# Kernel optimization log

Measured on AMD Instinct MI355X. Metric: run time of the kernel, lower is better.

The kernel has to match this reference:

```python
import jax, jax.numpy as jnp
import numpy as np

NORM_S = 3.0  # normalize_scale, learn_scale=False
NUM_CLASSES = 32


def setup_inputs() -> dict:
    key = jax.random.key(0)
    k1, k2 = jax.random.split(key)
    x = jax.random.normal(k1, (512, 128), dtype=jnp.float32)
    labels = jax.random.randint(k2, (512,), 0, NUM_CLASSES, dtype=jnp.int64)
    return {"x": x, "labels": labels}


def reference(x, labels):
    # L2-normalize rows and scale (MyTripletLoss.forward)
    f = NORM_S * x / jnp.linalg.norm(x, axis=1, keepdims=True)
    # pairwise squared distances, clamped at 0 (pairwise_distances)
    sq = jnp.sum(f * f, axis=1)
    D = jnp.clip(sq[:, None] + sq[None, :] - 2.0 * (f @ f.T), 0.0, None)  # [N,N]
    N = x.shape[0]
    # triplet_type == 0: valid triplet (i,j,k) iff i!=j, l_i==l_j, l_i!=l_k
    same = (labels[:, None] == labels[None, :]) & (~jnp.eye(N, dtype=bool))  # [i,j]
    diff = labels[:, None] != labels[None, :]                                # [i,k]
    mask = same[:, :, None] & diff[:, None, :]                               # [i,j,k]
    # DBL loss: log(1 + exp(D_ij - D_ik)) = softplus
    lt = jax.nn.softplus(D[:, :, None] - D[:, None, :])                      # [i,j,k]
    triplet_count = jnp.sum(mask).astype(lt.dtype)
    loss = jnp.sum(jnp.where(mask, lt, 0.0)) / triplet_count
    return loss.reshape(1)
```

## Files before the change

kernel.cpp:

```cpp
#include <hip/hip_runtime.h>
#include <math.h>

#define N 512
#define DIM 128
#define TT 32
#define PADS 132
#define NTRI (16 * 17 / 2)


__global__ void __launch_bounds__(256) gram_kernel(const float* __restrict__ x,
                                                   float* __restrict__ D) {
    __shared__ float xi[TT * PADS];
    __shared__ float xj[TT * PADS];
    __shared__ float rnA[TT];
    __shared__ float rnB[TT];

    int t = threadIdx.x;

    int b = blockIdx.x;
    int bi = (int)((sqrtf(8.0f * (float)b + 1.0f) - 1.0f) * 0.5f);
    while ((bi + 1) * (bi + 2) / 2 <= b) ++bi;
    while (bi * (bi + 1) / 2 > b) --bi;
    int bj = b - bi * (bi + 1) / 2;

    const float4* srcA = (const float4*)(x + bi * TT * DIM);
    const float4* srcB = (const float4*)(x + bj * TT * DIM);
    #pragma unroll
    for (int k = 0; k < (TT * DIM / 4) / 256; ++k) {
        int e = t + k * 256;
        int r = e >> 5, c4 = e & 31;
        *((float4*)(xi + r * PADS + 4 * c4)) = srcA[e];
        *((float4*)(xj + r * PADS + 4 * c4)) = srcB[e];
    }
    __syncthreads();

    {
        int quart = t & 3, r = t >> 2;
        const float* base = (r < TT) ? (xi + r * PADS) : (xj + (r - TT) * PADS);
        const float4* a = (const float4*)(base + quart * 32);
        float s0 = 0.0f, s1 = 0.0f;
        #pragma unroll
        for (int q = 0; q < 8; q += 2) {
            float4 a0 = a[q], a1 = a[q + 1];
            s0 += a0.x * a0.x + a0.y * a0.y + a0.z * a0.z + a0.w * a0.w;
            s1 += a1.x * a1.x + a1.y * a1.y + a1.z * a1.z + a1.w * a1.w;
        }
        float ss = s0 + s1;
        ss += __shfl_xor(ss, 1, 64);
        ss += __shfl_xor(ss, 2, 64);
        if (quart == 0) {
            if (r < TT) rnA[r] = rsqrtf(ss);
            else        rnB[r - TT] = rsqrtf(ss);
        }
    }
    __syncthreads();

    int tx = t & 15, ty = t >> 4;
    int i0 = 2 * ty, i1 = i0 + 1, j0 = 2 * tx, j1 = j0 + 1;
    float acc00 = 0.0f, acc01 = 0.0f, acc10 = 0.0f, acc11 = 0.0f;
    const float4* A0 = (const float4*)(xi + i0 * PADS);
    const float4* A1 = (const float4*)(xi + i1 * PADS);
    const float4* B0 = (const float4*)(xj + j0 * PADS);
    const float4* B1 = (const float4*)(xj + j1 * PADS);
    #pragma unroll 8
    for (int k4 = 0; k4 < DIM / 4; ++k4) {
        float4 a0 = A0[k4], a1 = A1[k4], b0 = B0[k4], b1 = B1[k4];
        acc00 += a0.x * b0.x + a0.y * b0.y + a0.z * b0.z + a0.w * b0.w;
        acc01 += a0.x * b1.x + a0.y * b1.y + a0.z * b1.z + a0.w * b1.w;
        acc10 += a1.x * b0.x + a1.y * b0.y + a1.z * b0.z + a1.w * b0.w;
        acc11 += a1.x * b1.x + a1.y * b1.y + a1.z * b1.z + a1.w * b1.w;
    }
    float ri0 = rnA[i0], ri1 = rnA[i1], rj0 = rnB[j0], rj1 = rnB[j1];
    float t00 = 18.0f * fmaxf(0.0f, 1.0f - acc00 * ri0 * rj0);
    float t01 = 18.0f * fmaxf(0.0f, 1.0f - acc01 * ri0 * rj1);
    float t10 = 18.0f * fmaxf(0.0f, 1.0f - acc10 * ri1 * rj0);
    float t11 = 18.0f * fmaxf(0.0f, 1.0f - acc11 * ri1 * rj1);

    {
        int gi0 = bi * TT + i0, gi1 = bi * TT + i1, gj = bj * TT + j0;
        float2 r0 = {t00, t01}, r1 = {t10, t11};
        *((float2*)(D + gi0 * N + gj)) = r0;
        *((float2*)(D + gi1 * N + gj)) = r1;
    }

    if (bi != bj) {
        __syncthreads();
        float* Tt = xi;
        Tt[j0 * 33 + i0] = t00;
        Tt[j1 * 33 + i0] = t01;
        Tt[j0 * 33 + i1] = t10;
        Tt[j1 * 33 + i1] = t11;
        __syncthreads();
        int ga0 = bj * TT + i0, ga1 = bj * TT + i1, gb = bi * TT + j0;
        float2 m0 = {Tt[i0 * 33 + j0], Tt[i0 * 33 + j1]};
        float2 m1 = {Tt[i1 * 33 + j0], Tt[i1 * 33 + j1]};
        *((float2*)(D + ga0 * N + gb)) = m0;
        *((float2*)(D + ga1 * N + gb)) = m1;
    }
}

__global__ void __launch_bounds__(256) loss_kernel(const float* __restrict__ Dm,
                                                   const int* __restrict__ labels,
                                                   float* __restrict__ sums,
                                                   float* __restrict__ cnts) {
    __shared__ int   lab[N];
    __shared__ float sameD[N];
    __shared__ float diffD[N];
    __shared__ float red[4];
    __shared__ int   nsame, ndiff;

    int i = blockIdx.x, t = threadIdx.x;
    lab[t]       = labels[t];
    lab[t + 256] = labels[t + 256];
    if (t == 0) { nsame = 0; ndiff = 0; }
    float d0 = Dm[i * N + t];
    float d1 = Dm[i * N + t + 256];
    __syncthreads();

    int li = lab[i];
    {
        int j = t;
        if (lab[j] == li) {
            if (j != i) { int p = atomicAdd(&nsame, 1); sameD[p] = d0; }
        } else { int p = atomicAdd(&ndiff, 1); diffD[p] = d0; }
        j = t + 256;
        if (lab[j] == li) {
            if (j != i) { int p = atomicAdd(&nsame, 1); sameD[p] = d1; }
        } else { int p = atomicAdd(&ndiff, 1); diffD[p] = d1; }
    }
    __syncthreads();

    int ns = nsame, nd = ndiff;
    float ek0 = (t < nd)       ? __expf(-diffD[t])       : 0.0f;
    float ek1 = (t + 256 < nd) ? __expf(-diffD[t + 256]) : 0.0f;
    float lsum = 0.0f;
    for (int js = 0; js < ns; ++js) {
        float es = __expf(sameD[js]);
        lsum += __logf(1.0f + es * ek0) + __logf(1.0f + es * ek1);
    }

    #pragma unroll
    for (int off = 32; off > 0; off >>= 1) lsum += __shfl_xor(lsum, off, 64);
    if ((t & 63) == 0) red[t >> 6] = lsum;
    __syncthreads();
    if (t == 0) {
        sums[i] = red[0] + red[1] + red[2] + red[3];
        cnts[i] = (float)(ns * nd);
    }
}

__global__ void __launch_bounds__(256) finalize_kernel(const float* __restrict__ sums,
                                                       const float* __restrict__ cnts,
                                                       float* __restrict__ out) {
    __shared__ float2 red[256];
    int t = threadIdx.x;
    float2 v;
    v.x = sums[t] + sums[t + 256];
    v.y = cnts[t] + cnts[t + 256];
    red[t] = v;
    __syncthreads();
    #pragma unroll
    for (int s = 128; s > 0; s >>= 1) {
        if (t < s) {
            red[t].x += red[t + s].x;
            red[t].y += red[t + s].y;
        }
        __syncthreads();
    }
    if (t == 0) out[0] = red[0].x / red[0].y;
}

extern "C" void kernel_launch(void* const* d_in, const int* in_sizes, int n_in,
                              void* d_out, int out_size, void* d_ws, size_t ws_size,
                              hipStream_t stream) {
    const float* x      = (const float*)d_in[0];
    const int*   labels = (const int*)d_in[1];
    float*       out    = (float*)d_out;

    float* Dm   = (float*)d_ws;
    float* sums = Dm + N * N;
    float* cnts = sums + N;

    gram_kernel<<<NTRI, 256, 0, stream>>>(x, Dm);
    loss_kernel<<<N, 256, 0, stream>>>(Dm, labels, sums, cnts);
    finalize_kernel<<<1, 256, 0, stream>>>(sums, cnts, out);
}
```

Measured before the change: 64.95 us.

## Use ballot-based compaction and precomputed exps in triplet loss kernel

Replaces the shared-memory atomic counters used to compact same- and different-label distances with wave ballots, popcounts and a small prefix over per-wave counts. It precomputes exp of the same-label distances once into shared memory instead of recomputing it in every thread's inner loop. The inner loop now uses log2 with a fused multiply-add and scales by ln2 once at the end. The gram kernel's thread-to-element mapping changes from adjacent pairs to strided rows and columns, with scalar stores replacing float2 stores. The compaction order becomes deterministic but needs extra barriers and shared buffers.

```diff
diff --git a/kernel.cpp b/kernel.cpp
--- a/kernel.cpp
+++ b/kernel.cpp
@@ -56,7 +56,7 @@
     __syncthreads();
 
     int tx = t & 15, ty = t >> 4;
-    int i0 = 2 * ty, i1 = i0 + 1, j0 = 2 * tx, j1 = j0 + 1;
+    int i0 = ty, i1 = ty + 16, j0 = tx, j1 = tx + 16;
     float acc00 = 0.0f, acc01 = 0.0f, acc10 = 0.0f, acc11 = 0.0f;
     const float4* A0 = (const float4*)(xi + i0 * PADS);
     const float4* A1 = (const float4*)(xi + i1 * PADS);
@@ -77,10 +77,12 @@
     float t11 = 18.0f * fmaxf(0.0f, 1.0f - acc11 * ri1 * rj1);
 
     {
-        int gi0 = bi * TT + i0, gi1 = bi * TT + i1, gj = bj * TT + j0;
-        float2 r0 = {t00, t01}, r1 = {t10, t11};
-        *((float2*)(D + gi0 * N + gj)) = r0;
-        *((float2*)(D + gi1 * N + gj)) = r1;
+        int gi0 = bi * TT + i0, gi1 = bi * TT + i1;
+        int gj0 = bj * TT + j0, gj1 = bj * TT + j1;
+        D[gi0 * N + gj0] = t00;
+        D[gi0 * N + gj1] = t01;
+        D[gi1 * N + gj0] = t10;
+        D[gi1 * N + gj1] = t11;
     }
 
     if (bi != bj) {
@@ -91,11 +93,14 @@
         Tt[j0 * 33 + i1] = t10;
         Tt[j1 * 33 + i1] = t11;
         __syncthreads();
-        int ga0 = bj * TT + i0, ga1 = bj * TT + i1, gb = bi * TT + j0;
-        float2 m0 = {Tt[i0 * 33 + j0], Tt[i0 * 33 + j1]};
-        float2 m1 = {Tt[i1 * 33 + j0], Tt[i1 * 33 + j1]};
-        *((float2*)(D + ga0 * N + gb)) = m0;
-        *((float2*)(D + ga1 * N + gb)) = m1;
+        float m00 = Tt[i0 * 33 + j0], m01 = Tt[i0 * 33 + j1];
+        float m10 = Tt[i1 * 33 + j0], m11 = Tt[i1 * 33 + j1];
+        int ga0 = bj * TT + i0, ga1 = bj * TT + i1;
+        int gb0 = bi * TT + j0, gb1 = bi * TT + j1;
+        D[ga0 * N + gb0] = m00;
+        D[ga0 * N + gb1] = m01;
+        D[ga1 * N + gb0] = m10;
+        D[ga1 * N + gb1] = m11;
     }
 }
 
@@ -106,38 +111,59 @@
     __shared__ int   lab[N];
     __shared__ float sameD[N];
     __shared__ float diffD[N];
+    __shared__ float esame[N];
+    __shared__ int   cS[8], cD[8];
     __shared__ float red[4];
-    __shared__ int   nsame, ndiff;
 
     int i = blockIdx.x, t = threadIdx.x;
     lab[t]       = labels[t];
     lab[t + 256] = labels[t + 256];
-    if (t == 0) { nsame = 0; ndiff = 0; }
     float d0 = Dm[i * N + t];
     float d1 = Dm[i * N + t + 256];
     __syncthreads();
 
     int li = lab[i];
-    {
-        int j = t;
-        if (lab[j] == li) {
-            if (j != i) { int p = atomicAdd(&nsame, 1); sameD[p] = d0; }
-        } else { int p = atomicAdd(&ndiff, 1); diffD[p] = d0; }
-        j = t + 256;
-        if (lab[j] == li) {
-            if (j != i) { int p = atomicAdd(&nsame, 1); sameD[p] = d1; }
-        } else { int p = atomicAdd(&ndiff, 1); diffD[p] = d1; }
-    }
-    __syncthreads();
-
-    int ns = nsame, nd = ndiff;
+    int lane = t & 63, w = t >> 6;
+    bool pS0 = (lab[t] == li) && (t != i);
+    bool pD0 = (lab[t] != li);
+    bool pS1 = (lab[t + 256] == li) && ((t + 256) != i);
+    bool pD1 = (lab[t + 256] != li);
+    unsigned long long bS0 = __ballot(pS0);
+    unsigned long long bD0 = __ballot(pD0);
+    unsigned long long bS1 = __ballot(pS1);
+    unsigned long long bD1 = __ballot(pD1);
+    if (lane == 0) {
+        cS[w]     = __popcll(bS0); cD[w]     = __popcll(bD0);
+        cS[w + 4] = __popcll(bS1); cD[w + 4] = __popcll(bD1);
+    }
+    __syncthreads();
+    int baseS0 = 0, baseD0 = 0, baseS1 = 0, baseD1 = 0, ns = 0, nd = 0;
+    #pragma unroll
+    for (int s = 0; s < 8; ++s) {
+        int cs = cS[s], cd = cD[s];
+        if (s < w)     { baseS0 += cs; baseD0 += cd; }
+        if (s < w + 4) { baseS1 += cs; baseD1 += cd; }
+        ns += cs; nd += cd;
+    }
+    unsigned long long lt = (1ull << lane) - 1ull;
+    if (pS0) sameD[baseS0 + __popcll(bS0 & lt)] = d0;
+    if (pD0) diffD[baseD0 + __popcll(bD0 & lt)] = d0;
+    if (pS1) sameD[baseS1 + __popcll(bS1 & lt)] = d1;
+    if (pD1) diffD[baseD1 + __popcll(bD1 & lt)] = d1;
+    __syncthreads();
+
+    if (t < ns)       esame[t]       = __expf(sameD[t]);
+    if (t + 256 < ns) esame[t + 256] = __expf(sameD[t + 256]);
+    __syncthreads();
+
     float ek0 = (t < nd)       ? __expf(-diffD[t])       : 0.0f;
     float ek1 = (t + 256 < nd) ? __expf(-diffD[t + 256]) : 0.0f;
     float lsum = 0.0f;
     for (int js = 0; js < ns; ++js) {
-        float es = __expf(sameD[js]);
-        lsum += __logf(1.0f + es * ek0) + __logf(1.0f + es * ek1);
-    }
+        float es = esame[js];
+        lsum += __log2f(fmaf(es, ek0, 1.0f)) + __log2f(fmaf(es, ek1, 1.0f));
+    }
+    lsum *= 0.6931471805599453f;
 
     #pragma unroll
     for (int off = 32; off > 0; off >>= 1) lsum += __shfl_xor(lsum, off, 64);
```

Measured after the change: 63.28 us. 1.03x faster.
